# Kernel tuning notes

Measured on AMD Instinct MI355X. Metric: run time of the kernel, lower is better.

## Reference

```python
import jax, jax.numpy as jnp
import numpy as np

DIM = 32
DEPTH = 2  # closed-form Lyndon-basis log-signature implemented for depth 2


def setup_inputs() -> dict:
    key = jax.random.key(0)
    B, L, D = 512, 2048, DIM
    x = jax.random.normal(key, (B, L, D), dtype=jnp.float32)
    return {"x": x}


def _logsig_depth2(x):
    # x: (B, L, D) batch of paths.
    dx = x[:, 1:, :] - x[:, :-1, :]                     # (B, L-1, D) increments
    prefix = jnp.cumsum(dx, axis=1)                      # inclusive prefix sums
    level1 = prefix[:, -1, :]                            # (B, D) total displacement
    prefix_excl = prefix - dx                            # prefix up to t-1 (exclusive)
    # level-2 signature S_ij = sum_t prefix_excl[t, i] * dx[t, j]  -> (B, D, D)
    S2 = jnp.einsum("bli,blj->bij", prefix_excl, dx)
    # log-signature level 2 = antisymmetric part (Levy areas), Lyndon words i<j
    A = 0.5 * (S2 - jnp.swapaxes(S2, 1, 2))             # (B, D, D)
    iu, ju = jnp.triu_indices(x.shape[-1], k=1)          # row-major upper triangle
    areas = A[:, iu, ju]                                 # (B, D*(D-1)/2)
    return jnp.concatenate([level1, areas], axis=-1)     # (B, D + D*(D-1)/2)


def reference(x):
    # Faithful batched equivalent of iisignature.logsig(path, prepare(dim, 2))
    # for every path in the batch (Lyndon basis, depth 2).
    return _logsig_depth2(x)
```

## Files before the change

### kernel.cpp

```cpp
#include <hip/hip_runtime.h>


constexpr int kB     = 512;
constexpr int kL     = 2048;
constexpr int kD     = 32;
constexpr int kOut   = 528;
constexpr int kNCH   = 4;
constexpr int kTper  = 512;

__global__ __launch_bounds__(256, 4)
void logsig_partial(const float* __restrict__ x, float* __restrict__ out) {
    __shared__ float sW[4][1024];
    __shared__ float sM[1024];
    __shared__ float sx0[32];
    __shared__ float sL1[32];

    const int b     = blockIdx.x >> 2;
    const int chunk = blockIdx.x & 3;
    const int tid   = threadIdx.x;
    const int wave  = tid >> 6;
    const int lane  = tid & 63;
    const int q     = lane >> 4;
    const int sub   = lane & 15;
    const int i0    = (sub >> 2) * 8;
    const int j0    = (sub & 3) * 8;

    const float* __restrict__ xb = x + (size_t)b * (kL * kD);

    const int t0   = chunk * kTper;
    const int tend = (t0 + kTper < kL - 1) ? (t0 + kTper) : (kL - 1);

    float acc[8][8];
    #pragma unroll
    for (int a = 0; a < 8; ++a)
        #pragma unroll
        for (int c = 0; c < 8; ++c) acc[a][c] = 0.0f;

    #pragma unroll 2
    for (int it = 0; it < kTper / 16; ++it) {
        const int t = t0 + it * 16 + wave * 4 + q;
        if (t < tend) {
            const float* row = xb + (size_t)t * kD;
            const float4 a0 = *(const float4*)(row + i0);
            const float4 a1 = *(const float4*)(row + i0 + 4);
            const float4 b0 = *(const float4*)(row + kD + j0);
            const float4 b1 = *(const float4*)(row + kD + j0 + 4);
            const float av[8] = {a0.x, a0.y, a0.z, a0.w, a1.x, a1.y, a1.z, a1.w};
            const float bv[8] = {b0.x, b0.y, b0.z, b0.w, b1.x, b1.y, b1.z, b1.w};
            #pragma unroll
            for (int a = 0; a < 8; ++a)
                #pragma unroll
                for (int c = 0; c < 8; ++c)
                    acc[a][c] += av[a] * bv[c];
        }
    }

    #pragma unroll
    for (int a = 0; a < 8; ++a)
        #pragma unroll
        for (int c = 0; c < 8; ++c) {
            float v = acc[a][c];
            v += __shfl_xor(v, 16, 64);
            v += __shfl_xor(v, 32, 64);
            acc[a][c] = v;
        }

    if (lane < 16) {
        #pragma unroll
        for (int a = 0; a < 8; ++a)
            #pragma unroll
            for (int c = 0; c < 8; ++c)
                sW[wave][(i0 + a) * 32 + (j0 + c)] = acc[a][c];
    }

    if (tid < 32) {
        const float x0v = xb[tid];
        sx0[tid] = x0v;
        sL1[tid] = xb[(size_t)(kL - 1) * kD + tid] - x0v;
    }
    __syncthreads();

    for (int cell = tid; cell < 1024; cell += 256)
        sM[cell] = sW[0][cell] + sW[1][cell] + sW[2][cell] + sW[3][cell];
    __syncthreads();

    float* ob = out + (size_t)b * kOut;
    for (int o = tid; o < kOut; o += 256) {
        if (o < 32) {
            if (chunk == 0) ob[o] = sL1[o];
        } else {
            int p = o - 32, i = 0;
            while (p >= 31 - i) { p -= 31 - i; ++i; }
            const int j = i + 1 + p;
            float v = 0.5f * (sM[i * 32 + j] - sM[j * 32 + i]);
            if (chunk == 0)
                v += 0.5f * (sx0[j] * sL1[i] - sx0[i] * sL1[j]);
            atomicAdd(ob + o, v);
        }
    }
}

extern "C" void kernel_launch(void* const* d_in, const int* in_sizes, int n_in,
                              void* d_out, int out_size, void* d_ws, size_t ws_size,
                              hipStream_t stream) {
    const float* x = (const float*)d_in[0];
    float* out = (float*)d_out;
    hipMemsetAsync(out, 0, (size_t)out_size * sizeof(float), stream);
    logsig_partial<<<dim3(kB * kNCH), dim3(256), 0, stream>>>(x, out);
}
```

Before: 221.3 us.

## Compute level-2 outer-product sums with split-bf16 MFMA via LDS-staged panels

Replaces the per-thread FP32 8x8 outer-product accumulation with MFMA 16x16x32 bf16 instructions. Each float is split into hi+lo bf16 parts and three MFMAs per tile approximate FP32 accuracy. Each wave now handles a contiguous 256-step window, staged through transposed LDS panels with register double-buffering. The grid shrinks from 4 to 2 blocks per batch, and partial results are reduced with LDS atomics. The bf16x3 split adds a small accuracy risk and some conversion overhead, but it moves the bulk FMA work onto matrix cores.

Measured after the change: 210.4 us. 4.9% less time.

```diff
diff --git a/kernel.cpp b/kernel.cpp
--- a/kernel.cpp
+++ b/kernel.cpp
@@ -1,99 +1,163 @@
 #include <hip/hip_runtime.h>
+#include <stdint.h>
 
 
 constexpr int kB     = 512;
 constexpr int kL     = 2048;
 constexpr int kD     = 32;
 constexpr int kOut   = 528;
-constexpr int kNCH   = 4;
-constexpr int kTper  = 512;
+constexpr int kTw    = 256;
+constexpr int kPan   = 32;
+constexpr int kSlot  = 36;
+
+typedef __attribute__((ext_vector_type(8))) short bfrag;
+typedef __attribute__((ext_vector_type(4))) float f4acc;
+
+union FragU { uint32_t u[4]; bfrag f; };
+
+__device__ __forceinline__ uint32_t bf16_rne(float f) {
+    uint32_t fb = __builtin_bit_cast(uint32_t, f);
+    return (fb + 0x7fffu + ((fb >> 16) & 1u)) >> 16;
+}
 
 __global__ __launch_bounds__(256, 4)
-void logsig_partial(const float* __restrict__ x, float* __restrict__ out) {
-    __shared__ float sW[4][1024];
-    __shared__ float sM[1024];
-    __shared__ float sx0[32];
-    __shared__ float sL1[32];
+void logsig_mfma(const float* __restrict__ x, float* __restrict__ out) {
+    __shared__ __align__(16) uint32_t xp[4][kD * kSlot];
+    __shared__ float sM[kD * kD];
+    __shared__ float sx0[kD], sL1[kD];
 
-    const int b     = blockIdx.x >> 2;
-    const int chunk = blockIdx.x & 3;
+    const int b     = blockIdx.x >> 1;
+    const int halfc = blockIdx.x & 1;
     const int tid   = threadIdx.x;
     const int wave  = tid >> 6;
     const int lane  = tid & 63;
-    const int q     = lane >> 4;
-    const int sub   = lane & 15;
-    const int i0    = (sub >> 2) * 8;
-    const int j0    = (sub & 3) * 8;
 
     const float* __restrict__ xb = x + (size_t)b * (kL * kD);
+    const int t0 = (halfc * 4 + wave) * kTw;
 
-    const int t0   = chunk * kTper;
-    const int tend = (t0 + kTper < kL - 1) ? (t0 + kTper) : (kL - 1);
+    uint32_t* wbuf = &xp[wave][0];
 
-    float acc[8][8];
+    const int srow = lane >> 3;
+    const int sd0  = (lane & 7) * 4;
+
+    f4acc acc[4];
     #pragma unroll
-    for (int a = 0; a < 8; ++a)
+    for (int t = 0; t < 4; ++t)
         #pragma unroll
-        for (int c = 0; c < 8; ++c) acc[a][c] = 0.0f;
+        for (int e = 0; e < 4; ++e) acc[t][e] = 0.0f;
 
-    #pragma unroll 2
-    for (int it = 0; it < kTper / 16; ++it) {
-        const int t = t0 + it * 16 + wave * 4 + q;
-        if (t < tend) {
-            const float* row = xb + (size_t)t * kD;
-            const float4 a0 = *(const float4*)(row + i0);
-            const float4 a1 = *(const float4*)(row + i0 + 4);
-            const float4 b0 = *(const float4*)(row + kD + j0);
-            const float4 b1 = *(const float4*)(row + kD + j0 + 4);
-            const float av[8] = {a0.x, a0.y, a0.z, a0.w, a1.x, a1.y, a1.z, a1.w};
-            const float bv[8] = {b0.x, b0.y, b0.z, b0.w, b1.x, b1.y, b1.z, b1.w};
-            #pragma unroll
-            for (int a = 0; a < 8; ++a)
+    auto load_panel = [&](int p, float4* G) {
+        #pragma unroll
+        for (int s = 0; s < 5; ++s) {
+            const int r = s * 8 + srow;
+            int row = t0 + p * kPan + r;
+            row = row < kL - 1 ? row : kL - 1;
+            if (r < 33)
+                G[s] = *(const float4*)(xb + (size_t)row * kD + sd0);
+        }
+    };
+
+    auto store_panel = [&](const float4* G) {
+        #pragma unroll
+        for (int s = 0; s < 5; ++s) {
+            const int r = s * 8 + srow;
+            if (r < 33) {
+                const float v[4] = {G[s].x, G[s].y, G[s].z, G[s].w};
                 #pragma unroll
-                for (int c = 0; c < 8; ++c)
-                    acc[a][c] += av[a] * bv[c];
+                for (int k = 0; k < 4; ++k) {
+                    const float f = v[k];
+                    const uint32_t hi = bf16_rne(f);
+                    const float fh = __builtin_bit_cast(float, hi << 16);
+                    const uint32_t lo = bf16_rne(f - fh);
+                    wbuf[(sd0 + k) * kSlot + r] = (hi & 0xffffu) | (lo << 16);
+                }
+            }
         }
+    };
+
+    const int m = lane & 15;
+    const int q = lane >> 4;
+
+    auto panel_compute = [&](void) {
+        const uint32_t* r0 = wbuf + m * kSlot + q * 8;
+        const uint32_t* r1 = wbuf + (m + 16) * kSlot + q * 8;
+        const uint4 a0l = *(const uint4*)(r0);
+        const uint4 a0h = *(const uint4*)(r0 + 4);
+        const uint4 a1l = *(const uint4*)(r1);
+        const uint4 a1h = *(const uint4*)(r1 + 4);
+        const uint32_t a0[8] = {a0l.x, a0l.y, a0l.z, a0l.w, a0h.x, a0h.y, a0h.z, a0h.w};
+        const uint32_t a1[8] = {a1l.x, a1l.y, a1l.z, a1l.w, a1h.x, a1h.y, a1h.z, a1h.w};
+        uint32_t b0[8], b1[8];
+        #pragma unroll
+        for (int j = 0; j < 8; ++j) { b0[j] = r0[j + 1]; b1[j] = r1[j + 1]; }
+
+        FragU A0H, A0L, A1H, A1L, B0H, B0L, B1H, B1L;
+        #pragma unroll
+        for (int j = 0; j < 4; ++j) {
+            A0H.u[j] = __builtin_amdgcn_perm(a0[2*j+1], a0[2*j], 0x05040100u);
+            A0L.u[j] = __builtin_amdgcn_perm(a0[2*j+1], a0[2*j], 0x07060302u);
+            A1H.u[j] = __builtin_amdgcn_perm(a1[2*j+1], a1[2*j], 0x05040100u);
+            A1L.u[j] = __builtin_amdgcn_perm(a1[2*j+1], a1[2*j], 0x07060302u);
+            B0H.u[j] = __builtin_amdgcn_perm(b0[2*j+1], b0[2*j], 0x05040100u);
+            B0L.u[j] = __builtin_amdgcn_perm(b0[2*j+1], b0[2*j], 0x07060302u);
+            B1H.u[j] = __builtin_amdgcn_perm(b1[2*j+1], b1[2*j], 0x05040100u);
+            B1L.u[j] = __builtin_amdgcn_perm(b1[2*j+1], b1[2*j], 0x07060302u);
+        }
+        acc[0] = __builtin_amdgcn_mfma_f32_16x16x32_bf16(A0H.f, B0H.f, acc[0], 0, 0, 0);
+        acc[0] = __builtin_amdgcn_mfma_f32_16x16x32_bf16(A0H.f, B0L.f, acc[0], 0, 0, 0);
+        acc[0] = __builtin_amdgcn_mfma_f32_16x16x32_bf16(A0L.f, B0H.f, acc[0], 0, 0, 0);
+        acc[1] = __builtin_amdgcn_mfma_f32_16x16x32_bf16(A0H.f, B1H.f, acc[1], 0, 0, 0);
+        acc[1] = __builtin_amdgcn_mfma_f32_16x16x32_bf16(A0H.f, B1L.f, acc[1], 0, 0, 0);
+        acc[1] = __builtin_amdgcn_mfma_f32_16x16x32_bf16(A0L.f, B1H.f, acc[1], 0, 0, 0);
+        acc[2] = __builtin_amdgcn_mfma_f32_16x16x32_bf16(A1H.f, B0H.f, acc[2], 0, 0, 0);
+        acc[2] = __builtin_amdgcn_mfma_f32_16x16x32_bf16(A1H.f, B0L.f, acc[2], 0, 0, 0);
+        acc[2] = __builtin_amdgcn_mfma_f32_16x16x32_bf16(A1L.f, B0H.f, acc[2], 0, 0, 0);
+        acc[3] = __builtin_amdgcn_mfma_f32_16x16x32_bf16(A1H.f, B1H.f, acc[3], 0, 0, 0);
+        acc[3] = __builtin_amdgcn_mfma_f32_16x16x32_bf16(A1H.f, B1L.f, acc[3], 0, 0, 0);
+        acc[3] = __builtin_amdgcn_mfma_f32_16x16x32_bf16(A1L.f, B1H.f, acc[3], 0, 0, 0);
+    };
+
+    float4 G[5];
+    load_panel(0, G);
+    store_panel(G);
+    for (int p = 0; p < kTw / kPan; ++p) {
+        float4 Gn[5];
+        if (p < kTw / kPan - 1) load_panel(p + 1, Gn);
+        panel_compute();
+        if (p < kTw / kPan - 1) store_panel(Gn);
     }
 
-    #pragma unroll
-    for (int a = 0; a < 8; ++a)
-        #pragma unroll
-        for (int c = 0; c < 8; ++c) {
-            float v = acc[a][c];
-            v += __shfl_xor(v, 16, 64);
-            v += __shfl_xor(v, 32, 64);
-            acc[a][c] = v;
-        }
-
-    if (lane < 16) {
-        #pragma unroll
-        for (int a = 0; a < 8; ++a)
-            #pragma unroll
-            for (int c = 0; c < 8; ++c)
-                sW[wave][(i0 + a) * 32 + (j0 + c)] = acc[a][c];
-    }
-
-    if (tid < 32) {
+    for (int c = tid; c < kD * kD; c += 256) sM[c] = 0.0f;
+    if (tid < kD) {
         const float x0v = xb[tid];
+        const float xev = xb[(size_t)(kL - 1) * kD + tid];
         sx0[tid] = x0v;
-        sL1[tid] = xb[(size_t)(kL - 1) * kD + tid] - x0v;
+        sL1[tid] = xev - x0v;
     }
     __syncthreads();
 
-    for (int cell = tid; cell < 1024; cell += 256)
-        sM[cell] = sW[0][cell] + sW[1][cell] + sW[2][cell] + sW[3][cell];
+    #pragma unroll
+    for (int t = 0; t < 4; ++t) {
+        const int tr = t >> 1, tc = t & 1;
+        #pragma unroll
+        for (int e = 0; e < 4; ++e) {
+            const int row = 16 * tr + q * 4 + e;
+            const int col = 16 * tc + m;
+            atomicAdd(&sM[row * kD + col], acc[t][e]);
+        }
+    }
     __syncthreads();
 
     float* ob = out + (size_t)b * kOut;
     for (int o = tid; o < kOut; o += 256) {
         if (o < 32) {
-            if (chunk == 0) ob[o] = sL1[o];
+            if (halfc == 0) ob[o] = sL1[o];
         } else {
             int p = o - 32, i = 0;
             while (p >= 31 - i) { p -= 31 - i; ++i; }
             const int j = i + 1 + p;
-            float v = 0.5f * (sM[i * 32 + j] - sM[j * 32 + i]);
-            if (chunk == 0)
+            float v = 0.5f * (sM[i * kD + j] - sM[j * kD + i]);
+            if (halfc == 0)
                 v += 0.5f * (sx0[j] * sL1[i] - sx0[i] * sL1[j]);
             atomicAdd(ob + o, v);
         }
@@ -106,5 +170,5 @@
     const float* x = (const float*)d_in[0];
     float* out = (float*)d_out;
     hipMemsetAsync(out, 0, (size_t)out_size * sizeof(float), stream);
-    logsig_partial<<<dim3(kB * kNCH), dim3(256), 0, stream>>>(x, out);
+    logsig_mfma<<<dim3(kB * 2), dim3(256), 0, stream>>>(x, out);
 }
```
